# Kernel optimization log

Measured on AMD Instinct MI355X. Metric: run time of the kernel, lower is better.

## Reference

```python
import jax, jax.numpy as jnp
import numpy as np

BN_EPS = 1e-5
L1_EPS = 1e-12


def setup_inputs() -> dict:
    key = jax.random.key(0)
    ks = jax.random.split(key, 3)
    T, N, F = 8, 256, 128
    node_feats = jax.random.normal(ks[0], (T, N, F), dtype=jnp.float32)
    # 1x1 conv weights, no bias: [out=F, in=2F]
    w1 = jax.random.normal(ks[1], (F, 2 * F), dtype=jnp.float32) * (1.0 / np.sqrt(2 * F))
    w2 = jax.random.normal(ks[2], (F, 2 * F), dtype=jnp.float32) * (1.0 / np.sqrt(2 * F))
    g1 = jnp.ones((F,), jnp.float32)
    b1 = jnp.zeros((F,), jnp.float32)
    g2 = jnp.ones((F,), jnp.float32)
    b2 = jnp.zeros((F,), jnp.float32)
    return {"node_feats": node_feats, "w1": w1, "g1": g1, "b1": b1,
            "w2": w2, "g2": g2, "b2": b2}


def _branch(x_ij, w, g, b):
    # 1x1 conv == per-pair matmul: [T,N,N,2F] @ [F,2F]^T -> [T,N,N,F]
    y = jnp.einsum('tnmc,fc->tnmf', x_ij, w)
    # BatchNorm2d (train mode): stats over batch and both spatial dims, biased var
    mean = jnp.mean(y, axis=(0, 1, 2))
    var = jnp.var(y, axis=(0, 1, 2))
    y = (y - mean) * jax.lax.rsqrt(var + BN_EPS) * g + b
    return jax.nn.relu(y)


def reference(node_feats, w1, g1, b1, w2, g2, b2):
    T, N, F = node_feats.shape
    # pairwise broadcast-concat: x_ij[t,i,j] = [x[t,i], x[t,j]]
    x_i = jnp.broadcast_to(node_feats[:, :, None, :], (T, N, N, F))
    x_j = jnp.broadcast_to(node_feats[:, None, :, :], (T, N, N, F))
    x_ij = jnp.concatenate([x_i, x_j], axis=-1)  # [T,N,N,2F]

    sim = _branch(x_ij, w1, g1, b1)[:, None]   # [T,1,N,N,F]
    dsim = _branch(x_ij, w2, g2, b2)[:, None]  # [T,1,N,N,F]
    edge = jnp.concatenate([sim, dsim], axis=1)  # [T,2,N,N,F]

    # zero the diagonal (i == j)
    diag_mask = (1.0 - jnp.eye(N, dtype=node_feats.dtype))[None, None, :, :, None]
    edge = edge * diag_mask

    # L1 normalize along last dim (F.normalize p=1)
    l1 = jnp.sum(jnp.abs(edge), axis=-1, keepdims=True)
    return edge / jnp.maximum(l1, L1_EPS)
```

## Files before the change

### kernel.cpp

```cpp
#include <hip/hip_runtime.h>


#define TT 8
#define NN 256
#define FF 128

typedef float vf4 __attribute__((ext_vector_type(4)));

__global__ __launch_bounds__(128) void k_matmul(
    const float* __restrict__ x,
    const float* __restrict__ w1,
    const float* __restrict__ w2,
    float* __restrict__ ws)
{
    __shared__ float xs[8][FF];
    const int tid = threadIdx.x;
    const int row0 = blockIdx.x * 8;

    {
        const float4* xv = (const float4*)(x + row0 * FF);
        ((float4*)xs)[tid]       = xv[tid];
        ((float4*)xs)[tid + 128] = xv[tid + 128];
    }
    __syncthreads();

    const int f = tid;
    float acc0[8], acc1[8], acc2[8], acc3[8];
    #pragma unroll
    for (int r = 0; r < 8; ++r) { acc0[r]=0.f; acc1[r]=0.f; acc2[r]=0.f; acc3[r]=0.f; }

    const float4* w1v = (const float4*)w1;
    const float4* w2v = (const float4*)w2;

    #pragma unroll 4
    for (int c4 = 0; c4 < 32; ++c4) {
        float4 qa1 = w1v[f * 64 + c4];
        float4 qb1 = w1v[f * 64 + 32 + c4];
        float4 qa2 = w2v[f * 64 + c4];
        float4 qb2 = w2v[f * 64 + 32 + c4];
        const int c = c4 * 4;
        #pragma unroll
        for (int r = 0; r < 8; ++r) {
            float x0 = xs[r][c], x1 = xs[r][c + 1], x2 = xs[r][c + 2], x3 = xs[r][c + 3];
            acc0[r] = fmaf(x0, qa1.x, fmaf(x1, qa1.y, fmaf(x2, qa1.z, fmaf(x3, qa1.w, acc0[r]))));
            acc1[r] = fmaf(x0, qb1.x, fmaf(x1, qb1.y, fmaf(x2, qb1.z, fmaf(x3, qb1.w, acc1[r]))));
            acc2[r] = fmaf(x0, qa2.x, fmaf(x1, qa2.y, fmaf(x2, qa2.z, fmaf(x3, qa2.w, acc2[r]))));
            acc3[r] = fmaf(x0, qb2.x, fmaf(x1, qb2.y, fmaf(x2, qb2.z, fmaf(x3, qb2.w, acc3[r]))));
        }
    }

    float* A1 = ws;
    float* B1 = ws + 262144;
    float* A2 = ws + 524288;
    float* B2 = ws + 786432;
    #pragma unroll
    for (int r = 0; r < 8; ++r) {
        int row = row0 + r;
        A1[row * FF + f] = acc0[r];
        B1[row * FF + f] = acc1[r];
        A2[row * FF + f] = acc2[r];
        B2[row * FF + f] = acc3[r];
    }

    {
        const int t  = row0 >> 8;
        const int n0 = row0 & 255;
        float* b1t = ws + 1048576 + (t * FF + f) * NN + n0;
        float* b2t = ws + 1310720 + (t * FF + f) * NN + n0;
        vf4 p0 = {acc1[0], acc1[1], acc1[2], acc1[3]};
        vf4 p1 = {acc1[4], acc1[5], acc1[6], acc1[7]};
        vf4 q0 = {acc3[0], acc3[1], acc3[2], acc3[3]};
        vf4 q1 = {acc3[4], acc3[5], acc3[6], acc3[7]};
        *(vf4*)(b1t)     = p0;
        *(vf4*)(b1t + 4) = p1;
        *(vf4*)(b2t)     = q0;
        *(vf4*)(b2t + 4) = q1;
    }
}

__global__ __launch_bounds__(256) void k_stats(
    const float* __restrict__ ab,
    float* __restrict__ sums, float* __restrict__ sumsq)
{
    const int bx = blockIdx.x;
    const int t = bx & 7, arr = bx >> 3;
    const float* A = ab + arr * 262144 + t * NN * FF;
    const int tid = threadIdx.x;
    const int f = tid & 127, h = tid >> 7;
    float s = 0.f, q = 0.f;
    for (int n = h; n < NN; n += 2) {
        float v = A[n * FF + f];
        s += v;
        q = fmaf(v, v, q);
    }
    __shared__ float ls[256], lq[256];
    ls[tid] = s; lq[tid] = q;
    __syncthreads();
    if (tid < 128) {
        sums [(arr * 8 + t) * FF + f] = ls[tid] + ls[tid + 128];
        sumsq[(arr * 8 + t) * FF + f] = lq[tid] + lq[tid + 128];
    }
}

__global__ __launch_bounds__(256) void k_scale(
    const float* __restrict__ sums, const float* __restrict__ sumsq,
    const float* __restrict__ g1, const float* __restrict__ b1,
    const float* __restrict__ g2, const float* __restrict__ b2,
    float* __restrict__ scale, float* __restrict__ bias)
{
    const int tid = threadIdx.x;
    const int br = tid >> 7, f = tid & 127;
    const int aA = 2 * br, aB = 2 * br + 1;
    float SA = 0.f, SB = 0.f, QA = 0.f, QB = 0.f, cross = 0.f;
    #pragma unroll
    for (int t = 0; t < TT; ++t) {
        float sa = sums[(aA * 8 + t) * FF + f];
        float sb = sums[(aB * 8 + t) * FF + f];
        SA += sa; SB += sb;
        cross = fmaf(sa, sb, cross);
        QA += sumsq[(aA * 8 + t) * FF + f];
        QB += sumsq[(aB * 8 + t) * FF + f];
    }
    const float invTN  = 1.0f / 2048.0f;
    const float invTNN = 1.0f / 262144.0f;
    float mA = SA * invTN, mB = SB * invTN;
    float m = mA + mB;
    float ey2 = (QA + QB) * invTN + cross * invTNN;
    float var = ey2 - m * m;
    float gf = br ? g2[f] : g1[f];
    float bf = br ? b2[f] : b1[f];
    float sc = gf * rsqrtf(var + 1e-5f);
    scale[br * FF + f] = sc;
    bias [br * FF + f] = bf - m * sc;
}

__global__ __launch_bounds__(256) void k_edge(
    const float* __restrict__ ws,
    const float* __restrict__ scale, const float* __restrict__ bias,
    float* __restrict__ out)
{
    const int bx = blockIdx.x;
    const int i  = bx & 255;
    const int br = (bx >> 8) & 1;
    const int t  = bx >> 9;
    const int tid = threadIdx.x;

    const float* A  = ws + (2 * br) * 262144 + (t * NN + i) * FF;
    const float* B  = ws + (2 * br + 1) * 262144 + t * NN * FF;
    const float* Bt = ws + 1048576 + br * 262144 + t * FF * NN;

    __shared__ float sc_lds[FF];
    __shared__ float cc_lds[FF];
    __shared__ vf4   part[4][NN / 4];
    __shared__ float r_lds[NN];

    if (tid < FF) {
        float sf = scale[br * FF + tid];
        float cf = fmaf(A[tid], sf, bias[br * FF + tid]);
        sc_lds[tid] = sf;
        cc_lds[tid] = cf;
    }
    __syncthreads();

    {
        const int jq = tid & 63;
        const int fq = tid >> 6;
        const float* bt = Bt + (fq * 32) * NN + jq * 4;
        float s0 = 0.f, s1 = 0.f, s2 = 0.f, s3 = 0.f;
        #pragma unroll 8
        for (int ff = 0; ff < 32; ++ff) {
            vf4 b = *(const vf4*)(bt + ff * NN);
            const int f = fq * 32 + ff;
            float sf = sc_lds[f];
            float cf = cc_lds[f];
            s0 += fmaxf(fmaf(b.x, sf, cf), 0.f);
            s1 += fmaxf(fmaf(b.y, sf, cf), 0.f);
            s2 += fmaxf(fmaf(b.z, sf, cf), 0.f);
            s3 += fmaxf(fmaf(b.w, sf, cf), 0.f);
        }
        vf4 p = {s0, s1, s2, s3};
        part[fq][jq] = p;
    }
    __syncthreads();
    {
        const float* p0 = (const float*)&part[0][0];
        const float* p1 = (const float*)&part[1][0];
        const float* p2 = (const float*)&part[2][0];
        const float* p3 = (const float*)&part[3][0];
        float l1 = p0[tid] + p1[tid] + p2[tid] + p3[tid];
        r_lds[tid] = 1.0f / fmaxf(l1, 1e-12f);
    }
    __syncthreads();

    const int wave = tid >> 6, lane = tid & 63;
    const int fo = (lane & 31) * 4;
    const int jh = lane >> 5;

    const vf4 s4 = *(const vf4*)(sc_lds + fo);
    const vf4 c4 = *(const vf4*)(cc_lds + fo);

    vf4* obase = (vf4*)(out + ((size_t)(t * 2 + br) * NN + i) * (size_t)NN * FF);

    #pragma unroll 4
    for (int jj = 0; jj < 32; ++jj) {
        const int j = wave * 64 + jj * 2 + jh;
        vf4 b = *(const vf4*)(B + j * FF + fo);
        float r = r_lds[j];
        r = (j == i) ? 0.0f : r;
        vf4 v;
        v.x = fmaxf(fmaf(b.x, s4.x, c4.x), 0.f) * r;
        v.y = fmaxf(fmaf(b.y, s4.y, c4.y), 0.f) * r;
        v.z = fmaxf(fmaf(b.z, s4.z, c4.z), 0.f) * r;
        v.w = fmaxf(fmaf(b.w, s4.w, c4.w), 0.f) * r;
        __builtin_nontemporal_store(v, &obase[(size_t)j * 32 + (lane & 31)]);
    }
}

extern "C" void kernel_launch(void* const* d_in, const int* in_sizes, int n_in,
                              void* d_out, int out_size, void* d_ws, size_t ws_size,
                              hipStream_t stream)
{
    const float* x  = (const float*)d_in[0];
    const float* w1 = (const float*)d_in[1];
    const float* g1 = (const float*)d_in[2];
    const float* b1 = (const float*)d_in[3];
    const float* w2 = (const float*)d_in[4];
    const float* g2 = (const float*)d_in[5];
    const float* b2 = (const float*)d_in[6];

    float* ws    = (float*)d_ws;
    float* sums  = ws + 1572864;
    float* sumsq = sums + 4096;
    float* scale = sumsq + 4096;
    float* bias  = scale + 256;
    float* out = (float*)d_out;

    k_matmul<<<256, 128, 0, stream>>>(x, w1, w2, ws);
    k_stats <<<32, 256, 0, stream>>>(ws, sums, sumsq);
    k_scale <<<1, 256, 0, stream>>>(sums, sumsq, g1, b1, g2, b2, scale, bias);
    k_edge  <<<4096, 256, 0, stream>>>(ws, scale, bias, out);
}
```

Before: 572.6 us.

## Compute L1 denominators in a separate register-tiled kernel before edge writes

Moves the per-(i,j) L1-norm reciprocal computation out of the output-writing kernel into a new k_denom kernel. There each thread accumulates four i rows against a column of B, so every B load is reused across several rows. It writes a reciprocal table into the workspace. The edge kernel then only loads that table row, zeroes the diagonal entry, and streams the output, which removes two barriers and the f-reduction from the store-bound kernel. In exchange it adds one kernel launch plus a 2M-float round trip through global memory.

```diff
diff --git a/kernel.cpp b/kernel.cpp
--- a/kernel.cpp
+++ b/kernel.cpp
@@ -134,9 +134,76 @@
     bias [br * FF + f] = bf - m * sc;
 }
 
+__global__ __launch_bounds__(256) void k_denom(
+    const float* __restrict__ ws,
+    const float* __restrict__ scale, const float* __restrict__ bias,
+    float* __restrict__ r)
+{
+    const int bx = blockIdx.x;
+    const int tb = bx >> 4;
+    const int i0 = (bx & 15) * 16;
+    const int br = tb & 1, t = tb >> 1;
+    const int tid = threadIdx.x;
+
+    const float* A  = ws + (2 * br) * 262144 + (t * NN + i0) * FF;
+    const float* Bt = ws + 1048576 + br * 262144 + t * FF * NN;
+
+    __shared__ float s_lds[FF];
+    __shared__ float c_lds[16][FF];
+
+    if (tid < FF) s_lds[tid] = scale[br * FF + tid];
+    #pragma unroll
+    for (int k = 0; k < 8; ++k) {
+        int idx = k * 256 + tid;
+        int f = idx & 127;
+        ((float*)c_lds)[idx] = fmaf(A[idx], scale[br * FF + f], bias[br * FF + f]);
+    }
+    __syncthreads();
+
+    const int jq = tid & 63, ig = tid >> 6;
+    vf4 z0 = {0,0,0,0}, z1 = z0, z2 = z0, z3 = z0;
+    const float* bt = Bt + jq * 4;
+
+    #pragma unroll 4
+    for (int f = 0; f < FF; ++f) {
+        vf4 b = *(const vf4*)(bt + f * NN);
+        float sf = s_lds[f];
+        vf4 d;
+        d.x = b.x * sf; d.y = b.y * sf; d.z = b.z * sf; d.w = b.w * sf;
+        float c0 = c_lds[ig * 4 + 0][f];
+        float c1 = c_lds[ig * 4 + 1][f];
+        float c2 = c_lds[ig * 4 + 2][f];
+        float c3 = c_lds[ig * 4 + 3][f];
+        z0.x += fmaxf(d.x + c0, 0.f); z0.y += fmaxf(d.y + c0, 0.f);
+        z0.z += fmaxf(d.z + c0, 0.f); z0.w += fmaxf(d.w + c0, 0.f);
+        z1.x += fmaxf(d.x + c1, 0.f); z1.y += fmaxf(d.y + c1, 0.f);
+        z1.z += fmaxf(d.z + c1, 0.f); z1.w += fmaxf(d.w + c1, 0.f);
+        z2.x += fmaxf(d.x + c2, 0.f); z2.y += fmaxf(d.y + c2, 0.f);
+        z2.z += fmaxf(d.z + c2, 0.f); z2.w += fmaxf(d.w + c2, 0.f);
+        z3.x += fmaxf(d.x + c3, 0.f); z3.y += fmaxf(d.y + c3, 0.f);
+        z3.z += fmaxf(d.z + c3, 0.f); z3.w += fmaxf(d.w + c3, 0.f);
+    }
+
+    float* rb = r + ((size_t)tb * NN + (i0 + ig * 4)) * NN + jq * 4;
+    vf4 o;
+    o.x = 1.0f / fmaxf(z0.x, 1e-12f); o.y = 1.0f / fmaxf(z0.y, 1e-12f);
+    o.z = 1.0f / fmaxf(z0.z, 1e-12f); o.w = 1.0f / fmaxf(z0.w, 1e-12f);
+    *(vf4*)(rb + 0 * NN) = o;
+    o.x = 1.0f / fmaxf(z1.x, 1e-12f); o.y = 1.0f / fmaxf(z1.y, 1e-12f);
+    o.z = 1.0f / fmaxf(z1.z, 1e-12f); o.w = 1.0f / fmaxf(z1.w, 1e-12f);
+    *(vf4*)(rb + 1 * NN) = o;
+    o.x = 1.0f / fmaxf(z2.x, 1e-12f); o.y = 1.0f / fmaxf(z2.y, 1e-12f);
+    o.z = 1.0f / fmaxf(z2.z, 1e-12f); o.w = 1.0f / fmaxf(z2.w, 1e-12f);
+    *(vf4*)(rb + 2 * NN) = o;
+    o.x = 1.0f / fmaxf(z3.x, 1e-12f); o.y = 1.0f / fmaxf(z3.y, 1e-12f);
+    o.z = 1.0f / fmaxf(z3.z, 1e-12f); o.w = 1.0f / fmaxf(z3.w, 1e-12f);
+    *(vf4*)(rb + 3 * NN) = o;
+}
+
 __global__ __launch_bounds__(256) void k_edge(
     const float* __restrict__ ws,
     const float* __restrict__ scale, const float* __restrict__ bias,
+    const float* __restrict__ r,
     float* __restrict__ out)
 {
     const int bx = blockIdx.x;
@@ -144,74 +211,45 @@
     const int br = (bx >> 8) & 1;
     const int t  = bx >> 9;
     const int tid = threadIdx.x;
-
-    const float* A  = ws + (2 * br) * 262144 + (t * NN + i) * FF;
-    const float* B  = ws + (2 * br + 1) * 262144 + t * NN * FF;
-    const float* Bt = ws + 1048576 + br * 262144 + t * FF * NN;
-
-    __shared__ float sc_lds[FF];
-    __shared__ float cc_lds[FF];
-    __shared__ vf4   part[4][NN / 4];
-    __shared__ float r_lds[NN];
-
-    if (tid < FF) {
-        float sf = scale[br * FF + tid];
-        float cf = fmaf(A[tid], sf, bias[br * FF + tid]);
-        sc_lds[tid] = sf;
-        cc_lds[tid] = cf;
-    }
-    __syncthreads();
-
-    {
-        const int jq = tid & 63;
-        const int fq = tid >> 6;
-        const float* bt = Bt + (fq * 32) * NN + jq * 4;
-        float s0 = 0.f, s1 = 0.f, s2 = 0.f, s3 = 0.f;
-        #pragma unroll 8
-        for (int ff = 0; ff < 32; ++ff) {
-            vf4 b = *(const vf4*)(bt + ff * NN);
-            const int f = fq * 32 + ff;
-            float sf = sc_lds[f];
-            float cf = cc_lds[f];
-            s0 += fmaxf(fmaf(b.x, sf, cf), 0.f);
-            s1 += fmaxf(fmaf(b.y, sf, cf), 0.f);
-            s2 += fmaxf(fmaf(b.z, sf, cf), 0.f);
-            s3 += fmaxf(fmaf(b.w, sf, cf), 0.f);
-        }
-        vf4 p = {s0, s1, s2, s3};
-        part[fq][jq] = p;
-    }
-    __syncthreads();
-    {
-        const float* p0 = (const float*)&part[0][0];
-        const float* p1 = (const float*)&part[1][0];
-        const float* p2 = (const float*)&part[2][0];
-        const float* p3 = (const float*)&part[3][0];
-        float l1 = p0[tid] + p1[tid] + p2[tid] + p3[tid];
-        r_lds[tid] = 1.0f / fmaxf(l1, 1e-12f);
-    }
-    __syncthreads();
-
     const int wave = tid >> 6, lane = tid & 63;
     const int fo = (lane & 31) * 4;
     const int jh = lane >> 5;
 
-    const vf4 s4 = *(const vf4*)(sc_lds + fo);
-    const vf4 c4 = *(const vf4*)(cc_lds + fo);
+    const float* A = ws + (2 * br) * 262144 + (t * NN + i) * FF;
+    const float* B = ws + (2 * br + 1) * 262144 + t * NN * FF;
+
+    __shared__ float r_lds[NN];
+
+    if (tid < 64) {
+        const vf4* rr = (const vf4*)(r + ((size_t)(t * 2 + br) * NN + i) * NN);
+        vf4 q = rr[tid];
+        if ((i >> 2) == tid) q[i & 3] = 0.0f;
+        ((vf4*)r_lds)[tid] = q;
+    }
+
+    const vf4 s4 = *(const vf4*)(scale + br * FF + fo);
+    const vf4 b4 = *(const vf4*)(bias  + br * FF + fo);
+    const vf4 a4 = *(const vf4*)(A + fo);
+    vf4 c4;
+    c4.x = fmaf(a4.x, s4.x, b4.x);
+    c4.y = fmaf(a4.y, s4.y, b4.y);
+    c4.z = fmaf(a4.z, s4.z, b4.z);
+    c4.w = fmaf(a4.w, s4.w, b4.w);
+
+    __syncthreads();
 
     vf4* obase = (vf4*)(out + ((size_t)(t * 2 + br) * NN + i) * (size_t)NN * FF);
 
-    #pragma unroll 4
+    #pragma unroll 8
     for (int jj = 0; jj < 32; ++jj) {
         const int j = wave * 64 + jj * 2 + jh;
         vf4 b = *(const vf4*)(B + j * FF + fo);
-        float r = r_lds[j];
-        r = (j == i) ? 0.0f : r;
+        float rv = r_lds[j];
         vf4 v;
-        v.x = fmaxf(fmaf(b.x, s4.x, c4.x), 0.f) * r;
-        v.y = fmaxf(fmaf(b.y, s4.y, c4.y), 0.f) * r;
-        v.z = fmaxf(fmaf(b.z, s4.z, c4.z), 0.f) * r;
-        v.w = fmaxf(fmaf(b.w, s4.w, c4.w), 0.f) * r;
+        v.x = fmaxf(fmaf(b.x, s4.x, c4.x), 0.f) * rv;
+        v.y = fmaxf(fmaf(b.y, s4.y, c4.y), 0.f) * rv;
+        v.z = fmaxf(fmaf(b.z, s4.z, c4.z), 0.f) * rv;
+        v.w = fmaxf(fmaf(b.w, s4.w, c4.w), 0.f) * rv;
         __builtin_nontemporal_store(v, &obase[(size_t)j * 32 + (lane & 31)]);
     }
 }
@@ -233,10 +271,12 @@
     float* sumsq = sums + 4096;
     float* scale = sumsq + 4096;
     float* bias  = scale + 256;
+    float* rr    = bias + 256;
     float* out = (float*)d_out;
 
     k_matmul<<<256, 128, 0, stream>>>(x, w1, w2, ws);
     k_stats <<<32, 256, 0, stream>>>(ws, sums, sumsq);
     k_scale <<<1, 256, 0, stream>>>(sums, sumsq, g1, b1, g2, b2, scale, bias);
-    k_edge  <<<4096, 256, 0, stream>>>(ws, scale, bias, out);
-}
+    k_denom <<<256, 256, 0, stream>>>(ws, scale, bias, rr);
+    k_edge  <<<4096, 256, 0, stream>>>(ws, scale, bias, rr, out);
+}
```

Result: slower. 602.8 us (+5.3%).
